# Kernel tuning notes

Hardware: AMD Instinct MI355X
Metric: run time of the kernel (lower is better)

Reference implementation:

```python
import jax, jax.numpy as jnp
import numpy as np

B, S, D, HD = 16, 2048, 1024, 64  # batch, seq, n_embd, head_dim


def setup_inputs() -> dict:
    key = jax.random.key(0)
    ks = jax.random.split(key, 4)
    std = 1.0 / np.sqrt(D)
    return {
        "x": jax.random.normal(ks[0], (B, S, D), dtype=jnp.float32),
        "Wq": jax.random.normal(ks[1], (D, HD), dtype=jnp.float32) * std,
        "bq": jnp.zeros((HD,), dtype=jnp.float32),
        "Wk": jax.random.normal(ks[2], (D, HD), dtype=jnp.float32) * std,
        "bk": jnp.zeros((HD,), dtype=jnp.float32),
        "Wv": jax.random.normal(ks[3], (D, HD), dtype=jnp.float32) * std,
        "bv": jnp.zeros((HD,), dtype=jnp.float32),
    }


def reference(x, Wq, bq, Wk, bk, Wv, bv):
    q = x @ Wq + bq  # [B,S,HD]
    k = x @ Wk + bk
    v = x @ Wv + bv
    scale = jnp.asarray(HD, x.dtype) ** -0.5
    scores = jnp.einsum("bqd,bkd->bqk", q, k) * scale  # [B,S,S]
    seq = x.shape[1]
    causal = jnp.tril(jnp.ones((seq, seq), dtype=bool))  # True = keep
    scores = jnp.where(causal, scores, jnp.asarray(-jnp.inf, scores.dtype))
    probs = jax.nn.softmax(scores, axis=-1)
    return jnp.einsum("bqk,bkd->bqd", probs, v)  # [B,S,HD]
```

## Files before the change

### kernel.cpp

```cpp
#include <hip/hip_runtime.h>
#include <hip/hip_bf16.h>
#include <math.h>

constexpr int Bsz  = 16;
constexpr int Seq  = 2048;
constexpr int Din  = 1024;
constexpr int Hd   = 64;
constexpr int Rows = Bsz * Seq;

typedef short  short8 __attribute__((ext_vector_type(8)));
typedef float  f32x4  __attribute__((ext_vector_type(4)));

__device__ __forceinline__ short bf16_bits(float f) {
    __hip_bfloat16 h = __float2bfloat16(f);
    return __builtin_bit_cast(short, h);
}

__global__ __launch_bounds__(256) void wt_prep(
    const float* __restrict__ Wq, const float* __restrict__ Wk,
    const float* __restrict__ Wv, short* __restrict__ Wf)
{
    const int u     = blockIdx.x * 256 + threadIdx.x;
    const int chunk = u / 768;
    const int rem   = u - chunk * 768;
    const int f     = rem >> 6;
    const int lane  = rem & 63;
    const int wg    = f >> 2, nt = f & 3;
    const int quad  = lane >> 4, l16 = lane & 15;
    const float* W  = (wg == 0) ? Wq : (wg == 1) ? Wk : Wv;
    const int k0 = chunk * 32 + quad * 8;
    const int n  = nt * 16 + l16;
    short8 v;
    #pragma unroll
    for (int j = 0; j < 8; ++j) v[j] = bf16_bits(W[(size_t)(k0 + j) * Hd + n]);
    *(short8*)(Wf + (size_t)u * 8) = v;
}

__global__ __launch_bounds__(256) void qkv_kernel(
    const float* __restrict__ x,
    const short* __restrict__ Wf,
    const float* __restrict__ bq, const float* __restrict__ bk,
    const float* __restrict__ bv,
    short* __restrict__ Qf, short* __restrict__ Kf, short* __restrict__ Vf)
{
    const int tid  = threadIdx.x;
    const int wave = tid >> 6;
    const int lane = tid & 63;
    const int quad = lane >> 4;
    const int l16  = lane & 15;
    const int bx   = blockIdx.x;
    const int m0   = bx * 64;

    const float* xrow = x + (size_t)(m0 + wave * 16 + l16) * Din + quad * 8;

    f32x4 acc[12] = {};

    #pragma unroll 2
    for (int c = 0; c < 32; ++c) {
        const float4 a0 = *(const float4*)(xrow + c * 32);
        const float4 a1 = *(const float4*)(xrow + c * 32 + 4);
        short8 af;
        af[0] = bf16_bits(a0.x); af[1] = bf16_bits(a0.y);
        af[2] = bf16_bits(a0.z); af[3] = bf16_bits(a0.w);
        af[4] = bf16_bits(a1.x); af[5] = bf16_bits(a1.y);
        af[6] = bf16_bits(a1.z); af[7] = bf16_bits(a1.w);
        const short* wsrc = Wf + (size_t)c * 6144 + lane * 8;
        #pragma unroll
        for (int f = 0; f < 12; ++f) {
            const short8 bb = *(const short8*)(wsrc + f * 512);
            acc[f] = __builtin_amdgcn_mfma_f32_16x16x32_bf16(af, bb, acc[f], 0, 0, 0);
        }
    }

    __shared__ __align__(16) short eS[4][2][16 * 72];
    __shared__ __align__(16) short eV[64 * 80];

    #pragma unroll
    for (int wg = 0; wg < 2; ++wg) {
        const float* bias = wg ? bk : bq;
        #pragma unroll
        for (int nt = 0; nt < 4; ++nt) {
            const float bb = bias[nt * 16 + l16];
            #pragma unroll
            for (int r = 0; r < 4; ++r)
                eS[wave][wg][(quad * 4 + r) * 72 + nt * 16 + l16] =
                    bf16_bits(acc[wg * 4 + nt][r] + bb);
        }
    }
    #pragma unroll
    for (int wg = 0; wg < 2; ++wg) {
        const short8 v0 = *(const short8*)&eS[wave][wg][l16 * 72 + quad * 8];
        const short8 v1 = *(const short8*)&eS[wave][wg][l16 * 72 + 32 + quad * 8];
        if (wg == 0) {
            const size_t tg = (size_t)bx * 4 + wave;
            *(short8*)(Qf + (tg * 2 + 0) * 512 + lane * 8) = v0;
            *(short8*)(Qf + (tg * 2 + 1) * 512 + lane * 8) = v1;
        } else {
            *(short8*)(Kf + (((size_t)bx * 2 + 0) * 4 + wave) * 512 + lane * 8) = v0;
            *(short8*)(Kf + (((size_t)bx * 2 + 1) * 4 + wave) * 512 + lane * 8) = v1;
        }
    }

    #pragma unroll
    for (int nt = 0; nt < 4; ++nt) {
        const float bb = bv[nt * 16 + l16];
        #pragma unroll
        for (int r = 0; r < 4; ++r)
            eV[(nt * 16 + l16) * 80 + wave * 16 + quad * 4 + r] =
                bf16_bits(acc[8 + nt][r] + bb);
    }
    __syncthreads();
    #pragma unroll
    for (int s = 0; s < 2; ++s) {
        const int slot   = tid + s * 256;
        const int lane_s = slot & 63;
        const int u      = slot >> 6;
        const int th     = u >> 2, ntd = u & 3;
        const int q_s    = lane_s >> 4, l_s = lane_s & 15;
        const short8 v = *(const short8*)&eV[(ntd * 16 + l_s) * 80 + th * 32 + q_s * 8];
        *(short8*)(Vf + (((size_t)bx * 2 + th) * 4 + ntd) * 512 + lane_s * 8) = v;
    }
}

__global__ __launch_bounds__(256) void attn_kernel(
    const short* __restrict__ Qf, const short* __restrict__ Kf,
    const short* __restrict__ Vf, float* __restrict__ out)
{
    const int tid  = threadIdx.x;
    const int wave = tid >> 6;
    const int lane = tid & 63;
    const int quad = lane >> 4;
    const int l16  = lane & 15;
    const int b    = blockIdx.y;
    const int bx   = blockIdx.x;
    const int qs   = (bx & 1) ? (127 - (bx >> 1)) : (bx >> 1);
    const int dTile = qs >> 2;
    const int tiles = dTile + 1;
    const int qoff  = (qs & 3) * 16;

    __shared__ __align__(16) unsigned char sm[17408 + 512];
    short* Ps   = (short*)sm;
    float* Obuf = (float*)sm;
    float* mb   = (float*)(sm + 17408);
    float* lb   = mb + 64;

    const size_t tg = (size_t)b * 128 + qs;
    const short8 qf0 = *(const short8*)(Qf + (tg * 2 + 0) * 512 + lane * 8);
    const short8 qf1 = *(const short8*)(Qf + (tg * 2 + 1) * 512 + lane * 8);

    f32x4 o[4] = {};
    float m_run[4], l_run[4];
    #pragma unroll
    for (int r = 0; r < 4; ++r) { m_run[r] = -INFINITY; l_run[r] = 0.0f; }

    const float C = 0.125f * 1.44269504088896340736f;

    for (int kt = wave; kt < tiles; kt += 4) {
        const short* ktile = Kf + (size_t)(b * 32 + kt) * 4096;
        const short* vtile = Vf + (size_t)(b * 32 + kt) * 4096;

        f32x4 s[4] = {};
        #pragma unroll
        for (int nt = 0; nt < 4; ++nt) {
            const short8 kf0 = *(const short8*)(ktile + ((0 * 4 + nt) * 64 + lane) * 8);
            const short8 kf1 = *(const short8*)(ktile + ((1 * 4 + nt) * 64 + lane) * 8);
            s[nt] = __builtin_amdgcn_mfma_f32_16x16x32_bf16(qf0, kf0, s[nt], 0, 0, 0);
            s[nt] = __builtin_amdgcn_mfma_f32_16x16x32_bf16(qf1, kf1, s[nt], 0, 0, 0);
        }

        if (kt == dTile) {
            #pragma unroll
            for (int nt = 0; nt < 4; ++nt) {
                const int kg = nt * 16 + l16;
                #pragma unroll
                for (int r = 0; r < 4; ++r) {
                    const int qg = qoff + quad * 4 + r;
                    s[nt][r] = (kg <= qg) ? s[nt][r] * C : -INFINITY;
                }
            }
        } else {
            #pragma unroll
            for (int nt = 0; nt < 4; ++nt)
                #pragma unroll
                for (int r = 0; r < 4; ++r) s[nt][r] *= C;
        }

        float rm[4];
        #pragma unroll
        for (int r = 0; r < 4; ++r)
            rm[r] = fmaxf(fmaxf(s[0][r], s[1][r]), fmaxf(s[2][r], s[3][r]));
        #pragma unroll
        for (int off = 1; off < 16; off <<= 1)
            #pragma unroll
            for (int r = 0; r < 4; ++r)
                rm[r] = fmaxf(rm[r], __shfl_xor(rm[r], off));

        float alpha[4];
        #pragma unroll
        for (int r = 0; r < 4; ++r) {
            const float mn = fmaxf(m_run[r], rm[r]);
            alpha[r] = exp2f(m_run[r] - mn);
            m_run[r] = mn;
        }

        float rs[4] = {0.f, 0.f, 0.f, 0.f};
        #pragma unroll
        for (int nt = 0; nt < 4; ++nt)
            #pragma unroll
            for (int r = 0; r < 4; ++r) {
                const float p = exp2f(s[nt][r] - m_run[r]);
                s[nt][r] = p;
                rs[r] += p;
            }
        #pragma unroll
        for (int off = 1; off < 16; off <<= 1)
            #pragma unroll
            for (int r = 0; r < 4; ++r)
                rs[r] += __shfl_xor(rs[r], off);
        #pragma unroll
        for (int r = 0; r < 4; ++r) l_run[r] = l_run[r] * alpha[r] + rs[r];

        #pragma unroll
        for (int r = 0; r < 4; ++r) {
            o[0][r] *= alpha[r]; o[1][r] *= alpha[r];
            o[2][r] *= alpha[r]; o[3][r] *= alpha[r];
        }

        #pragma unroll
        for (int nt = 0; nt < 4; ++nt)
            #pragma unroll
            for (int r = 0; r < 4; ++r)
                Ps[wave * 1152 + (quad * 4 + r) * 72 + nt * 16 + l16] = bf16_bits(s[nt][r]);

        const short8 pf0 = *(const short8*)&Ps[wave * 1152 + l16 * 72 + quad * 8];
        const short8 pf1 = *(const short8*)&Ps[wave * 1152 + l16 * 72 + 32 + quad * 8];

        #pragma unroll
        for (int nt = 0; nt < 4; ++nt) {
            const short8 vA = *(const short8*)(vtile + ((0 * 4 + nt) * 64 + lane) * 8);
            const short8 vB = *(const short8*)(vtile + ((1 * 4 + nt) * 64 + lane) * 8);
            o[nt] = __builtin_amdgcn_mfma_f32_16x16x32_bf16(pf0, vA, o[nt], 0, 0, 0);
            o[nt] = __builtin_amdgcn_mfma_f32_16x16x32_bf16(pf1, vB, o[nt], 0, 0, 0);
        }
    }

    if (l16 == 0) {
        #pragma unroll
        for (int r = 0; r < 4; ++r) mb[wave * 16 + quad * 4 + r] = m_run[r];
    }
    __syncthreads();

    float fac[4];
    #pragma unroll
    for (int r = 0; r < 4; ++r) {
        const int row = quad * 4 + r;
        const float mg = fmaxf(fmaxf(mb[row], mb[16 + row]),
                               fmaxf(mb[32 + row], mb[48 + row]));
        fac[r] = exp2f(m_run[r] - mg);
    }
    if (l16 == 0) {
        #pragma unroll
        for (int r = 0; r < 4; ++r) lb[wave * 16 + quad * 4 + r] = l_run[r] * fac[r];
    }
    #pragma unroll
    for (int nt = 0; nt < 4; ++nt)
        #pragma unroll
        for (int r = 0; r < 4; ++r)
            Obuf[wave * 1088 + (quad * 4 + r) * 68 + nt * 16 + l16] = o[nt][r] * fac[r];
    __syncthreads();

    {
        const int row = tid >> 4;
        const int c0  = (tid & 15) * 4;
        const float lsum = lb[row] + lb[16 + row] + lb[32 + row] + lb[48 + row];
        float4 a = *(const float4*)&Obuf[0 * 1088 + row * 68 + c0];
        const float4 a1 = *(const float4*)&Obuf[1 * 1088 + row * 68 + c0];
        const float4 a2 = *(const float4*)&Obuf[2 * 1088 + row * 68 + c0];
        const float4 a3 = *(const float4*)&Obuf[3 * 1088 + row * 68 + c0];
        a.x += a1.x + a2.x + a3.x;  a.y += a1.y + a2.y + a3.y;
        a.z += a1.z + a2.z + a3.z;  a.w += a1.w + a2.w + a3.w;
        const float inv = 1.0f / lsum;
        float4 r4 = make_float4(a.x * inv, a.y * inv, a.z * inv, a.w * inv);
        *(float4*)(out + ((size_t)b * Seq + qs * 16 + row) * Hd + c0) = r4;
    }
}

extern "C" void kernel_launch(void* const* d_in, const int* in_sizes, int n_in,
                              void* d_out, int out_size, void* d_ws, size_t ws_size,
                              hipStream_t stream)
{
    const float* x  = (const float*)d_in[0];
    const float* Wq = (const float*)d_in[1];
    const float* bq = (const float*)d_in[2];
    const float* Wk = (const float*)d_in[3];
    const float* bk = (const float*)d_in[4];
    const float* Wv = (const float*)d_in[5];
    const float* bv = (const float*)d_in[6];
    float* out = (float*)d_out;

    short* Qf = (short*)d_ws;
    short* Kf = Qf + (size_t)Rows * Hd;
    short* Vf = Kf + (size_t)Rows * Hd;
    short* Wf = Vf + (size_t)Rows * Hd;

    wt_prep<<<96, 256, 0, stream>>>(Wq, Wk, Wv, Wf);
    qkv_kernel<<<512, 256, 0, stream>>>(x, Wf, bq, bk, bv, Qf, Kf, Vf);
    attn_kernel<<<dim3(128, 16), 256, 0, stream>>>(Qf, Kf, Vf, out);
}
```

Before: 289.1 us.

## Double-buffer QKV weight chunks into LDS with async global_load_lds and prefetch x

The QKV projection now stages each weight chunk into a double-buffered LDS region with global_load_lds, overlapping the next chunk's load with the current MFMAs. The next x row slice is register-prefetched one iteration ahead. The epilogue's shared arrays are aliased onto the same buffer. The attention kernel also raises wave priority around its MFMA blocks with s_setprio, at the cost of a per-iteration __syncthreads in the projection loop.

```diff
diff --git a/kernel.cpp b/kernel.cpp
--- a/kernel.cpp
+++ b/kernel.cpp
@@ -14,6 +14,12 @@
 __device__ __forceinline__ short bf16_bits(float f) {
     __hip_bfloat16 h = __float2bfloat16(f);
     return __builtin_bit_cast(short, h);
+}
+
+typedef __attribute__((address_space(1))) const void gvoid_t;
+typedef __attribute__((address_space(3))) void lvoid_t;
+__device__ __forceinline__ void gll16(const void* g, void* l) {
+    __builtin_amdgcn_global_load_lds((gvoid_t*)g, (lvoid_t*)l, 16, 0, 0);
 }
 
 __global__ __launch_bounds__(256) void wt_prep(
@@ -51,29 +57,55 @@
     const int bx   = blockIdx.x;
     const int m0   = bx * 64;
 
+    __shared__ __align__(16) short smem[14336];
+    short* sW = smem;
+
     const float* xrow = x + (size_t)(m0 + wave * 16 + l16) * Din + quad * 8;
 
     f32x4 acc[12] = {};
 
-    #pragma unroll 2
+    {
+        const short* g = Wf + wave * 1536 + lane * 8;
+        short*       l = sW + wave * 1536;
+        gll16(g,        l);
+        gll16(g +  512, l +  512);
+        gll16(g + 1024, l + 1024);
+    }
+    float4 a0 = *(const float4*)(xrow);
+    float4 a1 = *(const float4*)(xrow + 4);
+    __syncthreads();
+
     for (int c = 0; c < 32; ++c) {
-        const float4 a0 = *(const float4*)(xrow + c * 32);
-        const float4 a1 = *(const float4*)(xrow + c * 32 + 4);
+        const int cur = (c & 1) * 6144;
+        if (c < 31) {
+            const short* g = Wf + (size_t)(c + 1) * 6144 + wave * 1536 + lane * 8;
+            short*       l = sW + (cur ^ 6144) + wave * 1536;
+            gll16(g,        l);
+            gll16(g +  512, l +  512);
+            gll16(g + 1024, l + 1024);
+        }
+        float4 b0 = a0, b1 = a1;
+        if (c < 31) {
+            b0 = *(const float4*)(xrow + (c + 1) * 32);
+            b1 = *(const float4*)(xrow + (c + 1) * 32 + 4);
+        }
         short8 af;
         af[0] = bf16_bits(a0.x); af[1] = bf16_bits(a0.y);
         af[2] = bf16_bits(a0.z); af[3] = bf16_bits(a0.w);
         af[4] = bf16_bits(a1.x); af[5] = bf16_bits(a1.y);
         af[6] = bf16_bits(a1.z); af[7] = bf16_bits(a1.w);
-        const short* wsrc = Wf + (size_t)c * 6144 + lane * 8;
+        const short* wsrc = sW + cur + lane * 8;
         #pragma unroll
         for (int f = 0; f < 12; ++f) {
             const short8 bb = *(const short8*)(wsrc + f * 512);
             acc[f] = __builtin_amdgcn_mfma_f32_16x16x32_bf16(af, bb, acc[f], 0, 0, 0);
         }
-    }
-
-    __shared__ __align__(16) short eS[4][2][16 * 72];
-    __shared__ __align__(16) short eV[64 * 80];
+        a0 = b0; a1 = b1;
+        __syncthreads();
+    }
+
+    short (*eS)[2][16 * 72] = reinterpret_cast<short(*)[2][16 * 72]>(smem);
+    short* eV = smem + 9216;
 
     #pragma unroll
     for (int wg = 0; wg < 2; ++wg) {
@@ -160,6 +192,7 @@
         const short* vtile = Vf + (size_t)(b * 32 + kt) * 4096;
 
         f32x4 s[4] = {};
+        __builtin_amdgcn_s_setprio(1);
         #pragma unroll
         for (int nt = 0; nt < 4; ++nt) {
             const short8 kf0 = *(const short8*)(ktile + ((0 * 4 + nt) * 64 + lane) * 8);
@@ -167,6 +200,7 @@
             s[nt] = __builtin_amdgcn_mfma_f32_16x16x32_bf16(qf0, kf0, s[nt], 0, 0, 0);
             s[nt] = __builtin_amdgcn_mfma_f32_16x16x32_bf16(qf1, kf1, s[nt], 0, 0, 0);
         }
+        __builtin_amdgcn_s_setprio(0);
 
         if (kt == dTile) {
             #pragma unroll
@@ -235,6 +269,7 @@
         const short8 pf0 = *(const short8*)&Ps[wave * 1152 + l16 * 72 + quad * 8];
         const short8 pf1 = *(const short8*)&Ps[wave * 1152 + l16 * 72 + 32 + quad * 8];
 
+        __builtin_amdgcn_s_setprio(1);
         #pragma unroll
         for (int nt = 0; nt < 4; ++nt) {
             const short8 vA = *(const short8*)(vtile + ((0 * 4 + nt) * 64 + lane) * 8);
@@ -242,6 +277,7 @@
             o[nt] = __builtin_amdgcn_mfma_f32_16x16x32_bf16(pf0, vA, o[nt], 0, 0, 0);
             o[nt] = __builtin_amdgcn_mfma_f32_16x16x32_bf16(pf1, vB, o[nt], 0, 0, 0);
         }
+        __builtin_amdgcn_s_setprio(0);
     }
 
     if (l16 == 0) {
```

New measurement: 275.4 us. 1.05x faster.
